# Kernel optimization log

Measured on AMD Instinct MI355X. Metric: run time of the kernel, lower is better.

## Reference

```python
import jax, jax.numpy as jnp
import numpy as np

NN_SIZE = 16
RADIUS2 = 0.5 * 0.5  # radius^2
EPS = 0.0001


def setup_inputs() -> dict:
    key = jax.random.key(0)
    points = jax.random.normal(key, (4, 8192, 3), dtype=jnp.float32)
    return {"points": points}


def reference(points):
    # points: (B, N, 3)
    B, N, C = points.shape
    # Brute-force KNN (pytorch3d ops.knn_points with K = nn_size + 1, self included)
    sq = jnp.sum(points * points, axis=-1)  # (B, N)
    d2_all = sq[:, :, None] + sq[:, None, :] - 2.0 * jnp.einsum('bnc,bmc->bnm', points, points)  # (B,N,N)
    _, idx = jax.lax.top_k(-d2_all, NN_SIZE + 1)  # smallest distances first, (B,N,K+1)
    knn_idx = idx[:, :, 1:]  # drop self, (B, N, K)
    # Gather neighbor coordinates; detached in the original (.detach())
    knn_points = jax.vmap(lambda p, i: p[i])(points, knn_idx)  # (B, N, K, 3)
    knn_points = jax.lax.stop_gradient(knn_points)
    # Recompute squared distances (as the module does)
    knn_v = knn_points - points[:, :, None, :]  # (B, N, K, 3)
    distance2 = jnp.sum(knn_v * knn_v, axis=-1)  # (B, N, K)
    loss = 1.0 / jnp.sqrt(distance2 + EPS)
    loss = jnp.where(distance2 < RADIUS2, loss, jnp.zeros_like(loss))
    # reduction == 'mean'
    return jnp.mean(loss)
```

## Files before the change

kernel.cpp:

```cpp
#include <hip/hip_runtime.h>

#define NPTS 8192
#define NBATCH 4
#define NTOT (NBATCH * NPTS)
#define NN 16
#define RAD2 0.25f
#define EPSF 1e-4f
#define BIGF 1e30f

#define GC 16
#define GP 18
#define CBS 6144
#define NCELL_TOT (NBATCH * CBS)

#define STHR 256
#define SWV 4
#define PPW 2
#define SNB (NTOT / (SWV * PPW))
#define HCAP 384

#define LOG2C 5.0103f
#define NCLAMP 257

#define WS_COUNTS 0
#define WS_RANGES (WS_COUNTS + NCELL_TOT * 4)
#define WS_CURSOR (WS_RANGES + NCELL_TOT * 8)
#define WS_SORTED (WS_CURSOR + NCELL_TOT * 4)
#define WS_BSUMS  (WS_SORTED + (NTOT + 64) * 16)
#define WS_NEEDED (WS_BSUMS + SNB * 4)

__device__ __forceinline__ int cellc(float v) {
  return min(max((int)floorf((v + 4.0f) * 2.0f), 0), GC - 1);
}

__device__ __forceinline__ float prsqrt(float x) {
  float r = __builtin_amdgcn_rsqf(x);
  r = r * fmaf(-0.5f * x * r, r, 1.5f);
  return r;
}

__device__ __forceinline__ int lanepre(unsigned long long m) {
  return __builtin_amdgcn_mbcnt_hi((unsigned)(m >> 32),
         __builtin_amdgcn_mbcnt_lo((unsigned)m, 0));
}

#define CE(a, b) { const float lo_ = fminf(a, b); const float hi_ = fmaxf(a, b); a = lo_; b = hi_; }


__global__ __launch_bounds__(256)
void zero_kernel(int* __restrict__ counts) {
  const int i = blockIdx.x * 256 + threadIdx.x;
  if (i < NCELL_TOT) counts[i] = 0;
}

__global__ __launch_bounds__(256)
void hist_kernel(const float* __restrict__ pts, int* __restrict__ counts) {
  const int i = blockIdx.x * 256 + threadIdx.x;
  if (i >= NTOT) return;
  const int b = i >> 13;
  const float x = pts[i * 3 + 0], y = pts[i * 3 + 1], z = pts[i * 3 + 2];
  const int c = b * CBS + ((cellc(z) + 1) * GP + (cellc(y) + 1)) * GP + (cellc(x) + 1);
  atomicAdd(&counts[c], 1);
}

__global__ __launch_bounds__(1024)
void scan_kernel(const int* __restrict__ counts, int2* __restrict__ ranges,
                 int* __restrict__ cursor) {
  __shared__ int wsum[16];
  __shared__ int woff[16];
  __shared__ int stot;
  const int b = blockIdx.x;
  const int tid = threadIdx.x;
  const int wid = tid >> 6;
  const int lane = tid & 63;
  const int g0 = b * CBS;
  int running = b * NPTS;
  for (int chunk = 0; chunk < CBS; chunk += 1024) {
    const int idx = chunk + tid;
    const int v = counts[g0 + idx];
    int x = v;
    for (int off = 1; off < 64; off <<= 1) {
      const int t = __shfl_up(x, off, 64);
      if (lane >= off) x += t;
    }
    if (lane == 63) wsum[wid] = x;
    __syncthreads();
    if (wid == 0) {
      int s = (lane < 16) ? wsum[lane] : 0;
      for (int off = 1; off < 16; off <<= 1) {
        const int t = __shfl_up(s, off, 64);
        if (lane >= off) s += t;
      }
      if (lane < 16) woff[lane] = s - wsum[lane];
      if (lane == 15) stot = s;
    }
    __syncthreads();
    const int excl = running + woff[wid] + x - v;
    ranges[g0 + idx] = make_int2(excl, v);
    cursor[g0 + idx] = excl;
    running += stot;
    __syncthreads();
  }
}

__global__ __launch_bounds__(256)
void scatter_kernel(const float* __restrict__ pts, int* __restrict__ cursor,
                    float4* __restrict__ sorted) {
  const int i = blockIdx.x * 256 + threadIdx.x;
  if (i >= NTOT) return;
  const int b = i >> 13;
  const float x = pts[i * 3 + 0], y = pts[i * 3 + 1], z = pts[i * 3 + 2];
  const int c = b * CBS + ((cellc(z) + 1) * GP + (cellc(y) + 1)) * GP + (cellc(x) + 1);
  const int pos = atomicAdd(&cursor[c], 1);
  sorted[pos] = make_float4(x, y, z, fmaf(x, x, fmaf(y, y, z * z)));
}


__device__ __forceinline__ int scan1(const float4* __restrict__ sorted,
    const int* rs, const int* re, float rr, int selfp,
    float m2x, float m2y, float m2z, float sp, float* __restrict__ hq, int lane) {
  int hcnt = 0;
#pragma unroll
  for (int m = 0; m < 9; ++m) {
    const int s = rs[m], e = re[m];
    for (int j0 = s; j0 < e; j0 += 64) {
      const int j = j0 + lane;
      float d2 = BIGF;
      if (j < e) {
        const float4 q = sorted[j];
        d2 = fmaf(q.x, m2x, fmaf(q.y, m2y, fmaf(q.z, m2z, q.w + sp)));
      }
      const bool hit = (d2 < rr) && (j != selfp);
      const unsigned long long bal = __ballot(hit);
      const int pos = hcnt + lanepre(bal & ((1ull << lane) - 1ull) ? bal & ((1ull << lane) - 1ull) : 0ull);
      const int pre = __popcll(bal & ((1ull << lane) - 1ull));
      const int p2 = hcnt + pre;
      if (hit && p2 < HCAP) hq[p2] = d2;
      hcnt += (int)__popcll(bal);
      (void)pos;
    }
  }
  return hcnt;
}

__device__ __forceinline__ void scan2(const float4* __restrict__ sorted,
    const int* rs, const int* re, float rr,
    int pA, float m2xA, float m2yA, float m2zA, float spA,
    int pB, float m2xB, float m2yB, float m2zB, float spB,
    float* __restrict__ hqA, float* __restrict__ hqB, int lane,
    int& hcntA, int& hcntB) {
  int hA = 0, hB = 0;
#pragma unroll
  for (int m = 0; m < 9; ++m) {
    const int s = rs[m], e = re[m];
    for (int j0 = s; j0 < e; j0 += 64) {
      const int j = j0 + lane;
      float d2A = BIGF, d2B = BIGF;
      if (j < e) {
        const float4 q = sorted[j];
        const float qw = q.w;
        d2A = fmaf(q.x, m2xA, fmaf(q.y, m2yA, fmaf(q.z, m2zA, qw + spA)));
        d2B = fmaf(q.x, m2xB, fmaf(q.y, m2yB, fmaf(q.z, m2zB, qw + spB)));
      }
      const unsigned long long below = (1ull << lane) - 1ull;
      const bool hitA = (d2A < rr) && (j != pA);
      const unsigned long long balA = __ballot(hitA);
      const int posA = hA + (int)__popcll(balA & below);
      if (hitA && posA < HCAP) hqA[posA] = d2A;
      hA += (int)__popcll(balA);
      const bool hitB = (d2B < rr) && (j != pB);
      const unsigned long long balB = __ballot(hitB);
      const int posB = hB + (int)__popcll(balB & below);
      if (hitB && posB < HCAP) hqB[posB] = d2B;
      hB += (int)__popcll(balB);
    }
  }
  hcntA = hA;
  hcntB = hB;
}

template<int R>
__device__ __forceinline__ float tourney(const float* __restrict__ hq, int hn, int lane) {
  float v[R];
#pragma unroll
  for (int r = 0; r < R; ++r) {
    const int idx = lane + 64 * r;
    v[r] = (idx < hn) ? hq[idx] : BIGF;
  }
  if constexpr (R == 3) { CE(v[0], v[1]); CE(v[1], v[2]); CE(v[0], v[1]); }
  if constexpr (R == 6) {
    CE(v[0], v[1]); CE(v[2], v[3]); CE(v[4], v[5]);
    CE(v[1], v[2]); CE(v[3], v[4]);
    CE(v[0], v[1]); CE(v[2], v[3]); CE(v[4], v[5]);
    CE(v[1], v[2]); CE(v[3], v[4]);
    CE(v[0], v[1]); CE(v[2], v[3]); CE(v[4], v[5]);
    CE(v[1], v[2]); CE(v[3], v[4]);
  }
  float loss = 0.0f;
#pragma unroll
  for (int r = 0; r < NN; ++r) {
    float g = v[0];
    g = fminf(g, __shfl_xor(g, 1));
    g = fminf(g, __shfl_xor(g, 2));
    g = fminf(g, __shfl_xor(g, 4));
    g = fminf(g, __shfl_xor(g, 8));
    g = fminf(g, __shfl_xor(g, 16));
    g = fminf(g, __shfl_xor(g, 32));
    loss += prsqrt(g + EPSF);
    const unsigned long long own = __ballot(v[0] == g);
    const int first = (int)(__ffsll((unsigned long long)own) - 1);
    if (lane == first) {
#pragma unroll
      for (int r2 = 0; r2 < R - 1; ++r2) v[r2] = v[r2 + 1];
      v[R - 1] = BIGF;
    }
  }
  return loss;
}

__device__ __forceinline__ float extract_loss(const float* __restrict__ hq, int hn, int lane) {
  if (hn <= 64) {
    float v = (lane < hn) ? hq[lane] : BIGF;
#pragma unroll
    for (int k = 2; k <= 64; k <<= 1) {
#pragma unroll
      for (int j = k >> 1; j > 0; j >>= 1) {
        const float o = __shfl_xor(v, j, 64);
        const bool keepmin = (((lane & j) == 0) != ((lane & k) != 0));
        v = keepmin ? fminf(v, o) : fmaxf(v, o);
      }
    }
    float l = (lane < NN && v < RAD2) ? prsqrt(v + EPSF) : 0.0f;
    l += __shfl_xor(l, 1);
    l += __shfl_xor(l, 2);
    l += __shfl_xor(l, 4);
    l += __shfl_xor(l, 8);
    l += __shfl_xor(l, 16);
    l += __shfl_xor(l, 32);
    return l;
  } else if (hn <= 192) {
    return tourney<3>(hq, hn, lane);
  }
  return tourney<6>(hq, hn, lane);
}


__global__ __launch_bounds__(STHR)
void search_kernel(const float4* __restrict__ sorted, const int2* __restrict__ rngs,
                   float* __restrict__ bsums) {
  __shared__ float hbuf[SWV][2][HCAP];
  __shared__ float wloss[SWV];

  const int tid = threadIdx.x;
  const int wv = tid >> 6;
  const int lane = tid & 63;
  const int p0 = (blockIdx.x * SWV + wv) * 2;
  const int p1 = p0 + 1;
  const int bb = p0 >> 13;

  const float4 ptA = sorted[p0];
  const float4 ptB = sorted[p1];
  const float m2xA = -2.0f * ptA.x, m2yA = -2.0f * ptA.y, m2zA = -2.0f * ptA.z;
  const float spA = ptA.w;
  const float m2xB = -2.0f * ptB.x, m2yB = -2.0f * ptB.y, m2zB = -2.0f * ptB.z;
  const float spB = ptB.w;

  const int rbA = __builtin_amdgcn_readfirstlane(
      bb * CBS + ((cellc(ptA.z) + 1) * GP + (cellc(ptA.y) + 1)) * GP);
  const int rbB = __builtin_amdgcn_readfirstlane(
      bb * CBS + ((cellc(ptB.z) + 1) * GP + (cellc(ptB.y) + 1)) * GP);
  const int xA = __builtin_amdgcn_readfirstlane(cellc(ptA.x));
  const int xB = __builtin_amdgcn_readfirstlane(cellc(ptB.x));

  const int rowoff[9] = {
    (-1 * GP - 1) * GP, (-1 * GP + 0) * GP, (-1 * GP + 1) * GP,
    ( 0 * GP - 1) * GP, ( 0 * GP + 0) * GP, ( 0 * GP + 1) * GP,
    ( 1 * GP - 1) * GP, ( 1 * GP + 0) * GP, ( 1 * GP + 1) * GP };

  float* hqA = hbuf[wv][0];
  float* hqB = hbuf[wv][1];
  int hnA, hnB;

  if (rbA == rbB) {
    const int lo = min(xA, xB);
    const int hi = max(xA, xB) + 2;
    int rs[9], re[9], ncand = 0;
#pragma unroll
    for (int m = 0; m < 9; ++m) {
      const int base = rbA + rowoff[m];
      const int2 a = rngs[base + lo];
      const int2 b = rngs[base + hi];
      rs[m] = a.x;
      re[m] = b.x + b.y;
      ncand += re[m] - rs[m];
    }
    const bool clamped = (ncand <= NCLAMP);
    float r0sq = RAD2;
    if (!clamped) r0sq = exp2f((LOG2C - log2f((float)ncand)) * (2.0f / 3.0f));

    int hA, hB;
    scan2(sorted, rs, re, r0sq, p0, m2xA, m2yA, m2zA, spA,
          p1, m2xB, m2yB, m2zB, spB, hqA, hqB, lane, hA, hB);
    hnA = min(hA, HCAP);
    hnB = min(hB, HCAP);
    if (hnA < NN && !clamped)
      hnA = min(scan1(sorted, rs, re, RAD2, p0, m2xA, m2yA, m2zA, spA, hqA, lane), HCAP);
    if (hnB < NN && !clamped)
      hnB = min(scan1(sorted, rs, re, RAD2, p1, m2xB, m2yB, m2zB, spB, hqB, lane), HCAP);
  } else {
    int rsA[9], reA[9], ncA = 0, rsB[9], reB[9], ncB = 0;
#pragma unroll
    for (int m = 0; m < 9; ++m) {
      const int baseA = rbA + rowoff[m];
      const int2 a0 = rngs[baseA + xA];
      const int2 a1 = rngs[baseA + xA + 2];
      rsA[m] = a0.x; reA[m] = a1.x + a1.y; ncA += reA[m] - rsA[m];
      const int baseB = rbB + rowoff[m];
      const int2 b0 = rngs[baseB + xB];
      const int2 b1 = rngs[baseB + xB + 2];
      rsB[m] = b0.x; reB[m] = b1.x + b1.y; ncB += reB[m] - rsB[m];
    }
    const bool clA = (ncA <= NCLAMP);
    const bool clB = (ncB <= NCLAMP);
    float rA = RAD2, rB = RAD2;
    if (!clA) rA = exp2f((LOG2C - log2f((float)ncA)) * (2.0f / 3.0f));
    if (!clB) rB = exp2f((LOG2C - log2f((float)ncB)) * (2.0f / 3.0f));
    hnA = min(scan1(sorted, rsA, reA, rA, p0, m2xA, m2yA, m2zA, spA, hqA, lane), HCAP);
    if (hnA < NN && !clA)
      hnA = min(scan1(sorted, rsA, reA, RAD2, p0, m2xA, m2yA, m2zA, spA, hqA, lane), HCAP);
    hnB = min(scan1(sorted, rsB, reB, rB, p1, m2xB, m2yB, m2zB, spB, hqB, lane), HCAP);
    if (hnB < NN && !clB)
      hnB = min(scan1(sorted, rsB, reB, RAD2, p1, m2xB, m2yB, m2zB, spB, hqB, lane), HCAP);
  }

  const float lossA = extract_loss(hqA, hnA, lane);
  const float lossB = extract_loss(hqB, hnB, lane);

  if (lane == 0) wloss[wv] = lossA + lossB;
  __syncthreads();
  if (tid == 0) {
    float s = 0.0f;
#pragma unroll
    for (int w = 0; w < SWV; ++w) s += wloss[w];
    bsums[blockIdx.x] = s;
  }
}

__global__ __launch_bounds__(256)
void finalize_kernel(const float* __restrict__ block_sums, int nblocks,
                     float* __restrict__ out) {
  __shared__ float s[256];
  float v = 0.0f;
  for (int idx = threadIdx.x; idx < nblocks; idx += 256) v += block_sums[idx];
  s[threadIdx.x] = v;
  __syncthreads();
  for (int off = 128; off > 0; off >>= 1) {
    if (threadIdx.x < off) s[threadIdx.x] += s[threadIdx.x + off];
    __syncthreads();
  }
  if (threadIdx.x == 0) out[0] = s[0] / (float)(NBATCH * NPTS * NN);
}


#define DTILE 1024
#define DNT 512
#define DNW 8
#define DNB (NTOT / 64)
#define CSTRIDE 17
#define QTRIG 13

__device__ __forceinline__ void insert16(float (&td)[NN], float& thrmax, float v) {
  if (v < thrmax) {
    bool done = false;
#pragma unroll
    for (int k = 0; k < NN; ++k) {
      const bool hit = (!done) && (td[k] == thrmax);
      if (hit) td[k] = v;
      done = done || hit;
    }
    thrmax = td[0];
#pragma unroll
    for (int k = 1; k < NN; ++k) thrmax = fmaxf(thrmax, td[k]);
  }
}

__device__ __forceinline__ void drain_queue(float* buf, int qbase, int& cnt,
                                            float (&td)[NN], float& thrmax) {
#pragma unroll
  for (int c = 0; c < 16; ++c) {
    const float v = (c < cnt) ? buf[qbase + c] : BIGF;
    insert16(td, thrmax, v);
  }
  cnt = 0;
}

__global__ __launch_bounds__(DNT)
void dense_kernel(const float* __restrict__ pts, float* __restrict__ block_sums) {
  __shared__ float4 tile[DTILE];
  __shared__ float buf[DNT * CSTRIDE];

  const int tid = threadIdx.x;
  const int wave = tid >> 6;
  const int lane = tid & 63;
  const int bid = blockIdx.x;
  const int b = bid / (NPTS / 64);
  const int base = (bid % (NPTS / 64)) * 64;
  const float* __restrict__ bp = pts + (size_t)b * NPTS * 3;

  const int i = base + lane;
  const float xi = bp[i * 3 + 0];
  const float yi = bp[i * 3 + 1];
  const float zi = bp[i * 3 + 2];

  float td[NN];
#pragma unroll
  for (int k = 0; k < NN; ++k) td[k] = BIGF;
  float thrmax = BIGF;
  int cnt = 0;
  const int qbase = tid * CSTRIDE;

  for (int tb = 0; tb < NPTS; tb += DTILE) {
    for (int pp = tid; pp < DTILE; pp += DNT) {
      const float* sp = bp + (size_t)(tb + pp) * 3;
      tile[pp] = make_float4(sp[0], sp[1], sp[2], 0.0f);
    }
    __syncthreads();
    const int jb = wave * (DTILE / DNW);
    for (int jj = 0; jj < DTILE / DNW; ++jj) {
      const float4 q = tile[jb + jj];
      const float ddx = q.x - xi, ddy = q.y - yi, ddz = q.z - zi;
      const float d2 = fmaf(ddx, ddx, fmaf(ddy, ddy, ddz * ddz));
      if (d2 < RAD2 && d2 != 0.0f) {
        buf[qbase + cnt] = d2;
        ++cnt;
      }
      if (__any(cnt >= QTRIG)) drain_queue(buf, qbase, cnt, td, thrmax);
    }
    __syncthreads();
  }
  drain_queue(buf, qbase, cnt, td, thrmax);
#pragma unroll
  for (int k = 0; k < NN; ++k) buf[qbase + k] = td[k];
  __syncthreads();

  if (wave == 0) {
    float sd[NN];
#pragma unroll
    for (int k = 0; k < NN; ++k) sd[k] = BIGF;
    float smax = BIGF;
    for (int w = 0; w < DNW; ++w) {
      for (int c = 0; c < NN; ++c) {
        insert16(sd, smax, buf[(w * 64 + lane) * CSTRIDE + c]);
      }
    }
    float loss = 0.0f;
#pragma unroll
    for (int k = 0; k < NN; ++k) {
      if (sd[k] < RAD2) loss += 1.0f / sqrtf(sd[k] + EPSF);
    }
    for (int off = 32; off > 0; off >>= 1) loss += __shfl_down(loss, off);
    if (lane == 0) block_sums[bid] = loss;
  }
}


extern "C" void kernel_launch(void* const* d_in, const int* in_sizes, int n_in,
                              void* d_out, int out_size, void* d_ws, size_t ws_size,
                              hipStream_t stream) {
  const float* pts = (const float*)d_in[0];
  float* out = (float*)d_out;
  char* ws = (char*)d_ws;

  if (ws_size >= (size_t)WS_NEEDED) {
    int* counts = (int*)(ws + WS_COUNTS);
    int2* rngs = (int2*)(ws + WS_RANGES);
    int* cursor = (int*)(ws + WS_CURSOR);
    float4* sorted = (float4*)(ws + WS_SORTED);
    float* bsums = (float*)(ws + WS_BSUMS);

    zero_kernel<<<(NCELL_TOT + 255) / 256, 256, 0, stream>>>(counts);
    hist_kernel<<<(NTOT + 255) / 256, 256, 0, stream>>>(pts, counts);
    scan_kernel<<<NBATCH, 1024, 0, stream>>>(counts, rngs, cursor);
    scatter_kernel<<<(NTOT + 255) / 256, 256, 0, stream>>>(pts, cursor, sorted);
    search_kernel<<<SNB, STHR, 0, stream>>>(sorted, rngs, bsums);
    finalize_kernel<<<1, 256, 0, stream>>>(bsums, SNB, out);
  } else {
    float* bsums = (float*)ws;
    dense_kernel<<<DNB, DNT, 0, stream>>>(pts, bsums);
    finalize_kernel<<<1, 256, 0, stream>>>(bsums, DNB, out);
  }
}
```

Measured before the change: 65.26 us.

## Single-pass scan, memset for count zeroing, and interleaved wave-to-pair mapping

The per-batch cell scan now gives each thread 6 consecutive counts and does a single block-wide prefix sum. This replaces the previous 6-chunk loop that needed three barriers per chunk. The zero kernel is replaced by hipMemsetAsync. The search kernel now assigns point pairs to waves strided by the block count, so each block mixes work from distant regions of the sorted order, which should even out per-block load. The ballot prefix code is also tidied and the lane mask hoisted out of the loop. The remapping changes memory locality between waves in a block and could hurt cache reuse of neighbouring cells.

```diff
diff --git a/kernel.cpp b/kernel.cpp
--- a/kernel.cpp
+++ b/kernel.cpp
@@ -39,19 +39,8 @@
   return r;
 }
 
-__device__ __forceinline__ int lanepre(unsigned long long m) {
-  return __builtin_amdgcn_mbcnt_hi((unsigned)(m >> 32),
-         __builtin_amdgcn_mbcnt_lo((unsigned)m, 0));
-}
-
 #define CE(a, b) { const float lo_ = fminf(a, b); const float hi_ = fmaxf(a, b); a = lo_; b = hi_; }
 
-
-__global__ __launch_bounds__(256)
-void zero_kernel(int* __restrict__ counts) {
-  const int i = blockIdx.x * 256 + threadIdx.x;
-  if (i < NCELL_TOT) counts[i] = 0;
-}
 
 __global__ __launch_bounds__(256)
 void hist_kernel(const float* __restrict__ pts, int* __restrict__ counts) {
@@ -66,40 +55,42 @@
 __global__ __launch_bounds__(1024)
 void scan_kernel(const int* __restrict__ counts, int2* __restrict__ ranges,
                  int* __restrict__ cursor) {
-  __shared__ int wsum[16];
+  __shared__ int wtot[16];
   __shared__ int woff[16];
-  __shared__ int stot;
   const int b = blockIdx.x;
   const int tid = threadIdx.x;
   const int wid = tid >> 6;
   const int lane = tid & 63;
-  const int g0 = b * CBS;
-  int running = b * NPTS;
-  for (int chunk = 0; chunk < CBS; chunk += 1024) {
-    const int idx = chunk + tid;
-    const int v = counts[g0 + idx];
-    int x = v;
-    for (int off = 1; off < 64; off <<= 1) {
-      const int t = __shfl_up(x, off, 64);
-      if (lane >= off) x += t;
-    }
-    if (lane == 63) wsum[wid] = x;
-    __syncthreads();
-    if (wid == 0) {
-      int s = (lane < 16) ? wsum[lane] : 0;
-      for (int off = 1; off < 16; off <<= 1) {
-        const int t = __shfl_up(s, off, 64);
-        if (lane >= off) s += t;
-      }
-      if (lane < 16) woff[lane] = s - wsum[lane];
-      if (lane == 15) stot = s;
-    }
-    __syncthreads();
-    const int excl = running + woff[wid] + x - v;
-    ranges[g0 + idx] = make_int2(excl, v);
-    cursor[g0 + idx] = excl;
-    running += stot;
-    __syncthreads();
+  const int g0 = b * CBS + tid * 6;
+
+  int v[6];
+  int lsum = 0;
+#pragma unroll
+  for (int k = 0; k < 6; ++k) { v[k] = counts[g0 + k]; lsum += v[k]; }
+
+  int x = lsum;
+  for (int off = 1; off < 64; off <<= 1) {
+    const int t = __shfl_up(x, off, 64);
+    if (lane >= off) x += t;
+  }
+  if (lane == 63) wtot[wid] = x;
+  __syncthreads();
+  if (wid == 0 && lane < 16) {
+    int s = wtot[lane];
+    for (int off = 1; off < 16; off <<= 1) {
+      const int t = __shfl_up(s, off, 64);
+      if (lane >= off) s += t;
+    }
+    woff[lane] = s - wtot[lane];
+  }
+  __syncthreads();
+
+  int run = b * NPTS + woff[wid] + (x - lsum);
+#pragma unroll
+  for (int k = 0; k < 6; ++k) {
+    ranges[g0 + k] = make_int2(run, v[k]);
+    cursor[g0 + k] = run;
+    run += v[k];
   }
 }
 
@@ -120,6 +111,7 @@
     const int* rs, const int* re, float rr, int selfp,
     float m2x, float m2y, float m2z, float sp, float* __restrict__ hq, int lane) {
   int hcnt = 0;
+  const unsigned long long below = (1ull << lane) - 1ull;
 #pragma unroll
   for (int m = 0; m < 9; ++m) {
     const int s = rs[m], e = re[m];
@@ -132,12 +124,9 @@
       }
       const bool hit = (d2 < rr) && (j != selfp);
       const unsigned long long bal = __ballot(hit);
-      const int pos = hcnt + lanepre(bal & ((1ull << lane) - 1ull) ? bal & ((1ull << lane) - 1ull) : 0ull);
-      const int pre = __popcll(bal & ((1ull << lane) - 1ull));
-      const int p2 = hcnt + pre;
-      if (hit && p2 < HCAP) hq[p2] = d2;
+      const int pos = hcnt + (int)__popcll(bal & below);
+      if (hit && pos < HCAP) hq[pos] = d2;
       hcnt += (int)__popcll(bal);
-      (void)pos;
     }
   }
   return hcnt;
@@ -150,6 +139,7 @@
     float* __restrict__ hqA, float* __restrict__ hqB, int lane,
     int& hcntA, int& hcntB) {
   int hA = 0, hB = 0;
+  const unsigned long long below = (1ull << lane) - 1ull;
 #pragma unroll
   for (int m = 0; m < 9; ++m) {
     const int s = rs[m], e = re[m];
@@ -162,7 +152,6 @@
         d2A = fmaf(q.x, m2xA, fmaf(q.y, m2yA, fmaf(q.z, m2zA, qw + spA)));
         d2B = fmaf(q.x, m2xB, fmaf(q.y, m2yB, fmaf(q.z, m2zB, qw + spB)));
       }
-      const unsigned long long below = (1ull << lane) - 1ull;
       const bool hitA = (d2A < rr) && (j != pA);
       const unsigned long long balA = __ballot(hitA);
       const int posA = hA + (int)__popcll(balA & below);
@@ -254,7 +243,8 @@
   const int tid = threadIdx.x;
   const int wv = tid >> 6;
   const int lane = tid & 63;
-  const int p0 = (blockIdx.x * SWV + wv) * 2;
+  const int pair = wv * SNB + blockIdx.x;
+  const int p0 = pair * 2;
   const int p1 = p0 + 1;
   const int bb = p0 >> 13;
 
@@ -478,7 +468,7 @@
     float4* sorted = (float4*)(ws + WS_SORTED);
     float* bsums = (float*)(ws + WS_BSUMS);
 
-    zero_kernel<<<(NCELL_TOT + 255) / 256, 256, 0, stream>>>(counts);
+    hipMemsetAsync(counts, 0, NCELL_TOT * 4, stream);
     hist_kernel<<<(NTOT + 255) / 256, 256, 0, stream>>>(pts, counts);
     scan_kernel<<<NBATCH, 1024, 0, stream>>>(counts, rngs, cursor);
     scatter_kernel<<<(NTOT + 255) / 256, 256, 0, stream>>>(pts, cursor, sorted);
```

Measured after the change: 60.98 us. -6.6%, faster.
